# Kernel optimization log

Hardware: AMD Instinct MI355X
Metric: run time of the kernel (lower is better)

## Reference

```python
import jax, jax.numpy as jnp
import numpy as np
import math

EPS = 1e-15
R_CUT = 5.0
BERN_K = 16
FEAT = 128
N_ATOMS = 16384
N_EDGES = 100000
# log binomial(BERN_K-1, k) for the Bernstein radial basis
LOG_BINOM = np.array([math.lgamma(BERN_K) - math.lgamma(k + 1) - math.lgamma(BERN_K - k)
                      for k in range(BERN_K)], dtype=np.float32)


def swish(x, a, b):
    # learnable swish: a * x * sigmoid(b * x)
    return a * x * jax.nn.sigmoid(b * x)


def resmlp(x, W1, b1, W2, b2, Wout, aa, bb):
    # Residual( PreAct(lin1) -> PreAct(lin2) ) -> act -> Linear(no bias)
    h = swish(x, aa[0], bb[0]) @ W1.T + b1
    h = swish(h, aa[1], bb[1]) @ W2.T + b2
    y = x + h
    return swish(y, aa[2], bb[2]) @ Wout.T


def sph_harm(u, l):
    ux, uy, uz = u[:, 0], u[:, 1], u[:, 2]
    if l == 0:
        return jnp.ones((u.shape[0], 1), u.dtype)
    if l == 1:
        return jnp.stack([uy, uz, ux], axis=-1)
    s3 = 3.0 ** 0.5
    return jnp.stack([s3 * ux * uy, s3 * uy * uz, 0.5 * (3.0 * uz ** 2 - 1.0),
                      s3 * ux * uz, 0.5 * s3 * (ux ** 2 - uy ** 2)], axis=-1)


def bernstein_rho(r, gamma):
    # rho_k(r) = C(K-1,k) x^k (1-x)^(K-1-k) * f_cut(r), x = exp(-gamma r)
    k = jnp.arange(BERN_K, dtype=r.dtype)
    x = jnp.exp(-gamma * r)[:, None]                      # (E,1)
    bern = jnp.exp(jnp.asarray(LOG_BINOM)) * x ** k * (1.0 - x) ** (BERN_K - 1 - k)
    inside = r < R_CUT
    denom = jnp.where(inside, R_CUT ** 2 - r ** 2, 1.0)
    fcut = jnp.where(inside, jnp.exp(-r ** 2 / denom), 0.0)
    return bern * fcut[:, None]                           # (E,K)


def setup_inputs() -> dict:
    key = jax.random.key(0)
    ks = jax.random.split(key, 16)
    D, K = FEAT, BERN_K
    sc = 1.0 / (D ** 0.5)
    inp = {
        'xyz': jax.random.normal(ks[0], (N_ATOMS, 3), jnp.float32),
        'x_tilde': jax.random.normal(ks[1], (N_ATOMS, D), jnp.float32),
        'nbrs': jax.random.randint(ks[2], (N_EDGES, 2), 0, N_ATOMS),
        # 5 ResidualMLPs stacked: order [c, s, p, d, l]
        'W1': jax.random.normal(ks[3], (5, D, D), jnp.float32) * sc,
        'b1': jnp.zeros((5, D), jnp.float32),
        'W2': jax.random.normal(ks[4], (5, D, D), jnp.float32) * sc,
        'b2': jnp.zeros((5, D), jnp.float32),
        'Wout': jax.random.normal(ks[5], (5, D, D), jnp.float32) * sc,
        'act_a': jnp.ones((5, 3), jnp.float32),
        'act_b': jnp.full((5, 3), 1.702, jnp.float32),
        'G_s': jax.random.normal(ks[6], (D, K), jnp.float32) * (1.0 / K ** 0.5),
        'G_p': jax.random.normal(ks[7], (D, K), jnp.float32) * (1.0 / K ** 0.5),
        'G_d': jax.random.normal(ks[8], (D, K), jnp.float32) * (1.0 / K ** 0.5),
        'P_1': jax.random.normal(ks[9], (D, D), jnp.float32) * sc,
        'P_2': jax.random.normal(ks[10], (D, D), jnp.float32) * sc,
        'D_1': jax.random.normal(ks[11], (D, D), jnp.float32) * sc,
        'D_2': jax.random.normal(ks[12], (D, D), jnp.float32) * sc,
        'gamma': jnp.asarray(0.5, jnp.float32),
    }
    return inp


def reference(xyz, x_tilde, nbrs, W1, b1, W2, b2, Wout, act_a, act_b,
              G_s, G_p, G_d, P_1, P_2, D_1, D_2, gamma):
    N = xyz.shape[0]
    src = nbrs[:, 0]
    dst = nbrs[:, 1]
    r_ij = xyz[dst] - xyz[src]                            # (E,3)
    r = jnp.sqrt((r_ij ** 2 + EPS).sum(-1))               # stable norm, (E,)
    u = r_ij / r[:, None]
    rho = bernstein_rho(r, gamma)                         # (E,K)
    x_j = x_tilde[dst]                                    # (E,D)

    def mlp(x, i):
        return resmlp(x, W1[i], b1[i], W2[i], b2[i], Wout[i], act_a[i], act_b[i])

    c_term = mlp(x_tilde, 0)                              # (N,D)

    quants = []
    for i, (l, G) in enumerate([(0, G_s), (1, G_p), (2, G_d)]):
        y = sph_harm(u, l)                                # (E,M)
        # fused g_matmul: G @ (rho (x) y) -> (E,D,M), avoids (E,K,M) temp
        gm = jnp.einsum('dk,ek,em->edm', G, rho, y)
        feat = mlp(x_j, i + 1)                            # (E,D)
        per_nbr = feat[:, :, None] * gm                   # (E,D,M)
        quants.append(jax.ops.segment_sum(per_nbr, src, num_segments=N))

    def take_inner(q, M1, M2):
        t1 = jnp.einsum('ij,njm->nim', M1, q)
        t2 = jnp.einsum('ij,njm->nim', M2, q)
        return (t1 * t2).sum(-1)                          # (N,D)

    inp = c_term + quants[0][:, :, 0] \
        + take_inner(quants[1], P_1, P_2) + take_inner(quants[2], D_1, D_2)
    return mlp(inp, 4)
```

## Files before the change

kernel.cpp:

```cpp
#include <hip/hip_runtime.h>
#include <math.h>

#define D 128

typedef __attribute__((ext_vector_type(8))) short short8v;
typedef __attribute__((ext_vector_type(4))) float f32x4;
typedef __attribute__((ext_vector_type(4))) unsigned int uint4v;

__device__ __forceinline__ float fast_swish(float v, float a, float b) {
  float e = __builtin_amdgcn_exp2f(-1.4426950408889634f * (b * v));
  return a * v * __builtin_amdgcn_rcpf(1.0f + e);
}

__device__ __forceinline__ void bf16split_rne(float v, unsigned short& h, unsigned short& l) {
  unsigned int u = __float_as_uint(v);
  unsigned int rh = (u + 0x7FFFu + ((u >> 16) & 1u)) & 0xFFFF0000u;
  h = (unsigned short)(rh >> 16);
  float lf = v - __uint_as_float(rh);
  unsigned int u2 = __float_as_uint(lf);
  unsigned int rl = u2 + 0x7FFFu + ((u2 >> 16) & 1u);
  l = (unsigned short)(rl >> 16);
}

__device__ __forceinline__ void bf16split_fast(float v, unsigned short& h, unsigned short& l) {
  unsigned int u = __float_as_uint(v);
  h = (unsigned short)(u >> 16);
  float lf = v - __uint_as_float(u & 0xFFFF0000u);
  unsigned int u2 = __float_as_uint(lf);
  l = (unsigned short)((u2 + 0x7FFFu + ((u2 >> 16) & 1u)) >> 16);
}

__device__ __forceinline__ f32x4 mfma3(short8v ah, short8v al, short8v bh, short8v bl, f32x4 acc) {
  acc = __builtin_amdgcn_mfma_f32_16x16x32_bf16(al, bh, acc, 0, 0, 0);
  acc = __builtin_amdgcn_mfma_f32_16x16x32_bf16(ah, bl, acc, 0, 0, 0);
  acc = __builtin_amdgcn_mfma_f32_16x16x32_bf16(ah, bh, acc, 0, 0, 0);
  return acc;
}

template <bool SW>
__device__ __forceinline__ void stage16(const float* __restrict__ src, int lane,
                                        unsigned short* shHi, unsigned short* shLo,
                                        float a, float b) {
#pragma unroll
  for (int i = 0; i < 4; ++i) {
    int t = lane + 64 * i;
    int r = t >> 4, c = t & 15;
    const float4 v0 = *(const float4*)(src + r * D + c * 8);
    const float4 v1 = *(const float4*)(src + r * D + c * 8 + 4);
    float vv[8] = {v0.x, v0.y, v0.z, v0.w, v1.x, v1.y, v1.z, v1.w};
    unsigned int hw[4], lw[4];
#pragma unroll
    for (int jj = 0; jj < 4; ++jj) {
      float x0 = SW ? fast_swish(vv[2 * jj], a, b) : vv[2 * jj];
      float x1 = SW ? fast_swish(vv[2 * jj + 1], a, b) : vv[2 * jj + 1];
      unsigned short h0, l0, h1, l1;
      bf16split_fast(x0, h0, l0);
      bf16split_fast(x1, h1, l1);
      hw[jj] = (unsigned int)h0 | ((unsigned int)h1 << 16);
      lw[jj] = (unsigned int)l0 | ((unsigned int)l1 << 16);
    }
    int off = (c * 16) ^ ((r & 7) << 4);
    uint4v hv = {hw[0], hw[1], hw[2], hw[3]};
    uint4v lv = {lw[0], lw[1], lw[2], lw[3]};
    *(uint4v*)((char*)(shHi + r * D) + off) = hv;
    *(uint4v*)((char*)(shLo + r * D) + off) = lv;
  }
}

__global__ void prep_weights_kernel(const float* __restrict__ W1, const float* __restrict__ W2,
                                    const float* __restrict__ Wo, const float* __restrict__ P1,
                                    const float* __restrict__ P2, const float* __restrict__ D1,
                                    const float* __restrict__ D2, unsigned short* __restrict__ prep) {
  int t = blockIdx.x * 256 + threadIdx.x;
  if (t >= 19 * 2048) return;
  int m = t >> 11;
  int rem = t & 2047;
  int nt = rem >> 8;
  int kc = (rem >> 6) & 3;
  int lane = rem & 63;
  const float* src;
  if (m < 5) src = W1 + (size_t)m * 16384;
  else if (m < 10) src = W2 + (size_t)(m - 5) * 16384;
  else if (m < 15) src = Wo + (size_t)(m - 10) * 16384;
  else if (m == 15) src = P1;
  else if (m == 16) src = P2;
  else if (m == 17) src = D1;
  else src = D2;
  int row = nt * 16 + (lane & 15);
  int k0 = kc * 32 + (lane >> 4) * 8;
  unsigned int hw[4], lw[4];
#pragma unroll
  for (int jj = 0; jj < 4; ++jj) {
    unsigned short h0, l0, h1, l1;
    bf16split_rne(src[row * D + k0 + 2 * jj], h0, l0);
    bf16split_rne(src[row * D + k0 + 2 * jj + 1], h1, l1);
    hw[jj] = (unsigned int)h0 | ((unsigned int)h1 << 16);
    lw[jj] = (unsigned int)l0 | ((unsigned int)l1 << 16);
  }
  size_t chunk = (size_t)((nt * 4 + kc) * 64 + lane);
  uint4v hv = {hw[0], hw[1], hw[2], hw[3]};
  uint4v lv = {lw[0], lw[1], lw[2], lw[3]};
  *(uint4v*)(prep + (size_t)(2 * m) * 16384 + chunk * 8) = hv;
  *(uint4v*)(prep + (size_t)(2 * m + 1) * 16384 + chunk * 8) = lv;
}

__global__ __launch_bounds__(256) void resmlp_mfma(
    const float* __restrict__ xin, const unsigned short* __restrict__ prep,
    const float* __restrict__ b1b, const float* __restrict__ b2b,
    const float* __restrict__ act_a, const float* __restrict__ act_b,
    float* __restrict__ outbase, int branch_off, int n_atoms)
{
  __shared__ __align__(16) unsigned short shHi[64 * D];
  __shared__ __align__(16) unsigned short shLo[64 * D];
  const int lane = threadIdx.x & 63;
  const int wid = threadIdx.x >> 6;
  const int atom0 = blockIdx.x * 64;
  const int br = blockIdx.y + branch_off;
  const float* b1 = b1b + br * D;
  const float* b2 = b2b + br * D;
  const float a0 = act_a[br * 3 + 0], g0 = act_b[br * 3 + 0];
  const float a1 = act_a[br * 3 + 1], g1 = act_b[br * 3 + 1];
  const float a2 = act_a[br * 3 + 2], g2 = act_b[br * 3 + 2];
  float* out = outbase + (size_t)blockIdx.y * n_atoms * D;
  const float* x0 = xin + (size_t)atom0 * D;

  stage16<true>(x0 + wid * 16 * D, lane, shHi + wid * 16 * D, shLo + wid * 16 * D, a0, g0);
  __syncthreads();

  const int rl = lane & 15;
  const int q = lane >> 4;
  const int rowq = q * 4;
  const int nt0 = wid * 2;

  f32x4 acc[4][2];

#define GEMM_LAYER(mat)                                                        \
  do {                                                                         \
    const unsigned short* ph = prep + (size_t)(2 * (mat)) * 16384;             \
    const unsigned short* pl = prep + (size_t)(2 * (mat) + 1) * 16384;         \
    _Pragma("unroll") for (int mt = 0; mt < 4; ++mt)                           \
        _Pragma("unroll") for (int j = 0; j < 2; ++j)                          \
            acc[mt][j] = f32x4{0.f, 0.f, 0.f, 0.f};                            \
    _Pragma("unroll") for (int kc = 0; kc < 4; ++kc) {                         \
      int ci0 = (nt0 * 4 + kc) * 64 + lane;                                    \
      int ci1 = ((nt0 + 1) * 4 + kc) * 64 + lane;                              \
      short8v bh0 = *(const short8v*)(ph + (size_t)ci0 * 8);                   \
      short8v bl0 = *(const short8v*)(pl + (size_t)ci0 * 8);                   \
      short8v bh1 = *(const short8v*)(ph + (size_t)ci1 * 8);                   \
      short8v bl1 = *(const short8v*)(pl + (size_t)ci1 * 8);                   \
      int aoff = (kc * 64 + q * 16) ^ ((rl & 7) << 4);                         \
      _Pragma("unroll") for (int mt = 0; mt < 4; ++mt) {                       \
        short8v ah = *(const short8v*)((const char*)(shHi + (mt * 16 + rl) * D) + aoff); \
        short8v al = *(const short8v*)((const char*)(shLo + (mt * 16 + rl) * D) + aoff); \
        acc[mt][0] = mfma3(ah, al, bh0, bl0, acc[mt][0]);                      \
        acc[mt][1] = mfma3(ah, al, bh1, bl1, acc[mt][1]);                      \
      }                                                                        \
    }                                                                          \
  } while (0)

  GEMM_LAYER(br);
  __syncthreads();
#pragma unroll
  for (int j = 0; j < 2; ++j) {
    int col = (nt0 + j) * 16 + rl;
    float bv = b1[col];
#pragma unroll
    for (int mt = 0; mt < 4; ++mt)
#pragma unroll
      for (int r = 0; r < 4; ++r) {
        int row = mt * 16 + rowq + r;
        float s = fast_swish(acc[mt][j][r] + bv, a1, g1);
        unsigned short h, l;
        bf16split_fast(s, h, l);
        int off = (col * 2) ^ ((row & 7) << 4);
        *(unsigned short*)((char*)(shHi + row * D) + off) = h;
        *(unsigned short*)((char*)(shLo + row * D) + off) = l;
      }
  }
  __syncthreads();

  GEMM_LAYER(5 + br);
  __syncthreads();
#pragma unroll
  for (int j = 0; j < 2; ++j) {
    int col = (nt0 + j) * 16 + rl;
    float bv = b2[col];
#pragma unroll
    for (int mt = 0; mt < 4; ++mt)
#pragma unroll
      for (int r = 0; r < 4; ++r) {
        int row = mt * 16 + rowq + r;
        float y = x0[row * D + col] + acc[mt][j][r] + bv;
        float s = fast_swish(y, a2, g2);
        unsigned short h, l;
        bf16split_fast(s, h, l);
        int off = (col * 2) ^ ((row & 7) << 4);
        *(unsigned short*)((char*)(shHi + row * D) + off) = h;
        *(unsigned short*)((char*)(shLo + row * D) + off) = l;
      }
  }
  __syncthreads();

  GEMM_LAYER(10 + br);
#pragma unroll
  for (int j = 0; j < 2; ++j)
#pragma unroll
    for (int mt = 0; mt < 4; ++mt)
#pragma unroll
      for (int r = 0; r < 4; ++r)
        out[(size_t)(atom0 + mt * 16 + rowq + r) * D + (nt0 + j) * 16 + rl] = acc[mt][j][r];
#undef GEMM_LAYER
}

__global__ __launch_bounds__(256) void inner_mfma(
    const float* __restrict__ q1, const float* __restrict__ q2,
    const unsigned short* __restrict__ prep,
    float* __restrict__ pA, float* __restrict__ pB, int n_atoms)
{
  __shared__ __align__(16) unsigned short shHi[64 * D];
  __shared__ __align__(16) unsigned short shLo[64 * D];
  const int lane = threadIdx.x & 63;
  const int wid = threadIdx.x >> 6;
  const int atom0 = blockIdx.x * 64;
  const int g = blockIdx.y;
  const size_t nd = (size_t)n_atoms * D;
  const int rl = lane & 15;
  const int q = lane >> 4;
  const int rowq = q * 4;
  const int nt0 = wid * 2;

  f32x4 eacc[4][2];
#pragma unroll
  for (int mt = 0; mt < 4; ++mt)
#pragma unroll
    for (int j = 0; j < 2; ++j) eacc[mt][j] = f32x4{0.f, 0.f, 0.f, 0.f};

  for (int pp = 0; pp < 2; ++pp) {
    const int part = g * 2 + pp;
    const float* qp = (part < 3) ? q1 + (size_t)part * nd : q2 + (size_t)(part - 3) * nd;
    const int m1 = (part < 3) ? 15 : 17;
    if (pp) __syncthreads();
    stage16<false>(qp + (size_t)atom0 * D + wid * 16 * D, lane,
                   shHi + wid * 16 * D, shLo + wid * 16 * D, 0.f, 0.f);
    __syncthreads();
    const unsigned short* p1h = prep + (size_t)(2 * m1) * 16384;
    const unsigned short* p1l = prep + (size_t)(2 * m1 + 1) * 16384;
    const unsigned short* p2h = prep + (size_t)(2 * m1 + 2) * 16384;
    const unsigned short* p2l = prep + (size_t)(2 * m1 + 3) * 16384;
#pragma unroll
    for (int j = 0; j < 2; ++j) {
      f32x4 t1[4], t2[4];
#pragma unroll
      for (int mt = 0; mt < 4; ++mt) {
        t1[mt] = f32x4{0.f, 0.f, 0.f, 0.f};
        t2[mt] = f32x4{0.f, 0.f, 0.f, 0.f};
      }
#pragma unroll
      for (int kc = 0; kc < 4; ++kc) {
        int ci = ((nt0 + j) * 4 + kc) * 64 + lane;
        short8v b1h = *(const short8v*)(p1h + (size_t)ci * 8);
        short8v b1l = *(const short8v*)(p1l + (size_t)ci * 8);
        short8v b2h = *(const short8v*)(p2h + (size_t)ci * 8);
        short8v b2l = *(const short8v*)(p2l + (size_t)ci * 8);
        int aoff = (kc * 64 + q * 16) ^ ((rl & 7) << 4);
#pragma unroll
        for (int mt = 0; mt < 4; ++mt) {
          short8v ah = *(const short8v*)((const char*)(shHi + (mt * 16 + rl) * D) + aoff);
          short8v al = *(const short8v*)((const char*)(shLo + (mt * 16 + rl) * D) + aoff);
          t1[mt] = mfma3(ah, al, b1h, b1l, t1[mt]);
          t2[mt] = mfma3(ah, al, b2h, b2l, t2[mt]);
        }
      }
#pragma unroll
      for (int mt = 0; mt < 4; ++mt) eacc[mt][j] += t1[mt] * t2[mt];
    }
  }

  float* outp = (g < 3) ? (pA + (size_t)g * nd) : pB;
#pragma unroll
  for (int j = 0; j < 2; ++j)
#pragma unroll
    for (int mt = 0; mt < 4; ++mt)
#pragma unroll
      for (int r = 0; r < 4; ++r)
        outp[(size_t)(atom0 + mt * 16 + rowq + r) * D + (nt0 + j) * 16 + rl] = eacc[mt][j][r];
}

__global__ void edge_geom_kernel(const float* __restrict__ xyz,
                                 const int* __restrict__ nbrs,
                                 const float* __restrict__ gamma_p,
                                 float* __restrict__ rho_ws,
                                 float* __restrict__ y_ws, int n_edges)
{
  int e = blockIdx.x * 256 + threadIdx.x;
  if (e >= n_edges) return;
  int s = nbrs[2 * e], dd = nbrs[2 * e + 1];
  float rx = xyz[3 * dd + 0] - xyz[3 * s + 0];
  float ry = xyz[3 * dd + 1] - xyz[3 * s + 1];
  float rz = xyz[3 * dd + 2] - xyz[3 * s + 2];
  float r2 = rx * rx + ry * ry + rz * rz + 3e-15f;
  float r = sqrtf(r2);
  float inv = 1.0f / r;
  float ux = rx * inv, uy = ry * inv, uz = rz * inv;
  float gamma = gamma_p[0];
  float xv = __expf(-gamma * r);
  float omx = 1.0f - xv;
  float fcut = 0.0f;
  if (r < 5.0f) fcut = __expf(-r2 / (25.0f - r2));
  float xp[16], op[16];
  xp[0] = 1.f; op[0] = 1.f;
#pragma unroll
  for (int k = 1; k < 16; ++k) { xp[k] = xp[k - 1] * xv; op[k] = op[k - 1] * omx; }
  const float C[16] = {1.f, 15.f, 105.f, 455.f, 1365.f, 3003.f, 5005.f, 6435.f,
                       6435.f, 5005.f, 3003.f, 1365.f, 455.f, 105.f, 15.f, 1.f};
  float* rp = rho_ws + (size_t)e * 16;
#pragma unroll
  for (int k = 0; k < 16; ++k) rp[k] = C[k] * xp[k] * op[15 - k] * fcut;
  const float s3 = 1.7320508075688772f;
  float* yp = y_ws + (size_t)e * 8;
  yp[0] = uy; yp[1] = uz; yp[2] = ux;
  yp[3] = s3 * ux * uy; yp[4] = s3 * uy * uz; yp[5] = 0.5f * (3.f * uz * uz - 1.f);
  yp[6] = s3 * ux * uz; yp[7] = 0.5f * s3 * (ux * ux - uy * uy);
}

__global__ void hist_kernel(const int* __restrict__ nbrs, int* __restrict__ counts, int n_edges) {
  int e = blockIdx.x * 256 + threadIdx.x;
  if (e < n_edges) atomicAdd(&counts[nbrs[2 * e]], 1);
}

__global__ __launch_bounds__(1024) void scan_kernel(const int* __restrict__ counts,
                                                    int* __restrict__ offsets, int n) {
  __shared__ int part[1024];
  int tid = threadIdx.x;
  int base = tid * 16;
  int loc[16]; int s = 0;
#pragma unroll
  for (int i = 0; i < 16; ++i) {
    int c = (base + i < n) ? counts[base + i] : 0;
    loc[i] = c; s += c;
  }
  part[tid] = s;
  __syncthreads();
  for (int off = 1; off < 1024; off <<= 1) {
    int v = (tid >= off) ? part[tid - off] : 0;
    __syncthreads();
    part[tid] += v;
    __syncthreads();
  }
  int run = (tid == 0) ? 0 : part[tid - 1];
#pragma unroll
  for (int i = 0; i < 16; ++i) {
    if (base + i < n) offsets[base + i] = run;
    run += loc[i];
  }
}

__global__ void scatter_kernel(const int* __restrict__ nbrs, const int* __restrict__ offsets,
                               int* __restrict__ cursor, int* __restrict__ sorted, int n_edges) {
  int e = blockIdx.x * 256 + threadIdx.x;
  if (e < n_edges) {
    int s = nbrs[2 * e];
    int pos = offsets[s] + atomicAdd(&cursor[s], 1);
    sorted[pos] = e;
  }
}

__global__ __launch_bounds__(128) void aggregate_kernel(
    const float* __restrict__ rho_ws, const float* __restrict__ y_ws,
    const int* __restrict__ nbrs, const int* __restrict__ offsets,
    const int* __restrict__ counts, const int* __restrict__ sorted,
    const float* __restrict__ feat1, const float* __restrict__ feat2,
    const float* __restrict__ feat3,
    const float* __restrict__ Gs, const float* __restrict__ Gp,
    const float* __restrict__ Gd,
    float* __restrict__ q0, float* __restrict__ q1, float* __restrict__ q2,
    int n_atoms)
{
  int n = blockIdx.x;
  int d = threadIdx.x;
  float gs[16], gp[16], gd[16];
#pragma unroll
  for (int c = 0; c < 4; ++c) {
    float4 v = *(const float4*)&Gs[d * 16 + 4 * c];
    gs[4 * c] = v.x; gs[4 * c + 1] = v.y; gs[4 * c + 2] = v.z; gs[4 * c + 3] = v.w;
    v = *(const float4*)&Gp[d * 16 + 4 * c];
    gp[4 * c] = v.x; gp[4 * c + 1] = v.y; gp[4 * c + 2] = v.z; gp[4 * c + 3] = v.w;
    v = *(const float4*)&Gd[d * 16 + 4 * c];
    gd[4 * c] = v.x; gd[4 * c + 1] = v.y; gd[4 * c + 2] = v.z; gd[4 * c + 3] = v.w;
  }
  float a0 = 0.f, a1[3] = {0.f, 0.f, 0.f}, a2[5] = {0.f, 0.f, 0.f, 0.f, 0.f};
  int off = offsets[n], cnt = counts[n];
  for (int i = 0; i < cnt; ++i) {
    int e = sorted[off + i];
    int dst = nbrs[2 * e + 1];
    const float4* rp = (const float4*)(rho_ws + (size_t)e * 16);
    float4 r0v = rp[0], r1v = rp[1], r2v = rp[2], r3v = rp[3];
    float rho[16] = {r0v.x, r0v.y, r0v.z, r0v.w, r1v.x, r1v.y, r1v.z, r1v.w,
                     r2v.x, r2v.y, r2v.z, r2v.w, r3v.x, r3v.y, r3v.z, r3v.w};
    const float4* ypv = (const float4*)(y_ws + (size_t)e * 8);
    float4 y0v = ypv[0], y1v = ypv[1];
    float g_s = 0.f, g_p = 0.f, g_d = 0.f;
#pragma unroll
    for (int k = 0; k < 16; ++k) {
      g_s += gs[k] * rho[k];
      g_p += gp[k] * rho[k];
      g_d += gd[k] * rho[k];
    }
    float f1 = feat1[(size_t)dst * D + d];
    float f2 = feat2[(size_t)dst * D + d];
    float f3 = feat3[(size_t)dst * D + d];
    a0 += f1 * g_s;
    float ap = f2 * g_p;
    a1[0] += ap * y0v.x; a1[1] += ap * y0v.y; a1[2] += ap * y0v.z;
    float ad = f3 * g_d;
    a2[0] += ad * y0v.w; a2[1] += ad * y1v.x; a2[2] += ad * y1v.y;
    a2[3] += ad * y1v.z; a2[4] += ad * y1v.w;
  }
  q0[(size_t)n * D + d] = a0;
#pragma unroll
  for (int m = 0; m < 3; ++m) q1[((size_t)m * n_atoms + n) * D + d] = a1[m];
#pragma unroll
  for (int m = 0; m < 5; ++m) q2[((size_t)m * n_atoms + n) * D + d] = a2[m];
}

__global__ void assemble_kernel(const float* __restrict__ cterm,
                                const float* __restrict__ q0,
                                const float* __restrict__ pA,
                                const float* __restrict__ pB,
                                float* __restrict__ inp, int nd4)
{
  int i = blockIdx.x * 256 + threadIdx.x;
  if (i >= nd4) return;
  const float4* c = (const float4*)cterm;
  const float4* z = (const float4*)q0;
  const float4* a = (const float4*)pA;
  const float4* b = (const float4*)pB;
  float4 v = c[i], zz = z[i];
  float4 a0 = a[i], a1 = a[i + (size_t)nd4], a2 = a[i + 2 * (size_t)nd4], bb = b[i];
  float4 r;
  r.x = v.x + zz.x + a0.x + a1.x + a2.x + bb.x;
  r.y = v.y + zz.y + a0.y + a1.y + a2.y + bb.y;
  r.z = v.z + zz.z + a0.z + a1.z + a2.z + bb.z;
  r.w = v.w + zz.w + a0.w + a1.w + a2.w + bb.w;
  ((float4*)inp)[i] = r;
}

extern "C" void kernel_launch(void* const* d_in, const int* in_sizes, int n_in,
                              void* d_out, int out_size, void* d_ws, size_t ws_size,
                              hipStream_t stream)
{
  const float* xyz     = (const float*)d_in[0];
  const float* x_tilde = (const float*)d_in[1];
  const int*   nbrs    = (const int*)d_in[2];
  const float* W1      = (const float*)d_in[3];
  const float* b1      = (const float*)d_in[4];
  const float* W2      = (const float*)d_in[5];
  const float* b2      = (const float*)d_in[6];
  const float* Wout    = (const float*)d_in[7];
  const float* act_a   = (const float*)d_in[8];
  const float* act_b   = (const float*)d_in[9];
  const float* Gs      = (const float*)d_in[10];
  const float* Gp      = (const float*)d_in[11];
  const float* Gd      = (const float*)d_in[12];
  const float* P1      = (const float*)d_in[13];
  const float* P2      = (const float*)d_in[14];
  const float* D1m     = (const float*)d_in[15];
  const float* D2m     = (const float*)d_in[16];
  const float* gamma   = (const float*)d_in[17];
  float* out = (float*)d_out;

  const int n_atoms = in_sizes[0] / 3;
  const int n_edges = in_sizes[2] / 2;

  float* ws = (float*)d_ws;
  size_t nd = (size_t)n_atoms * D;
  float* feats  = ws;
  float* q0     = feats + 4 * nd;
  float* q1     = q0 + nd;
  float* q2     = q1 + 3 * nd;
  float* rho_ws = q2 + 5 * nd;
  float* y_ws   = rho_ws + (size_t)n_edges * 16;
  float* inp    = y_ws + (size_t)n_edges * 8;
  int* counts  = (int*)(inp + nd);
  int* offsets = counts + n_atoms;
  int* cursor  = offsets + n_atoms;
  int* sorted  = cursor + n_atoms;
  unsigned short* prep =
      (unsigned short*)(((uintptr_t)(sorted + n_edges) + 15) & ~(uintptr_t)15);

  float* pA = feats + nd;
  float* pB = rho_ws;

  hipMemsetAsync(counts, 0, (size_t)n_atoms * sizeof(int), stream);
  hipMemsetAsync(cursor, 0, (size_t)n_atoms * sizeof(int), stream);

  dim3 blk(256);
  int eb = (n_edges + 255) / 256;

  prep_weights_kernel<<<(19 * 2048 + 255) / 256, blk, 0, stream>>>(
      W1, W2, Wout, P1, P2, D1m, D2m, prep);

  resmlp_mfma<<<dim3(n_atoms / 64, 4), dim3(256), 0, stream>>>(
      x_tilde, prep, b1, b2, act_a, act_b, feats, 0, n_atoms);

  edge_geom_kernel<<<eb, blk, 0, stream>>>(xyz, nbrs, gamma, rho_ws, y_ws, n_edges);
  hist_kernel<<<eb, blk, 0, stream>>>(nbrs, counts, n_edges);
  scan_kernel<<<1, 1024, 0, stream>>>(counts, offsets, n_atoms);
  scatter_kernel<<<eb, blk, 0, stream>>>(nbrs, offsets, cursor, sorted, n_edges);

  aggregate_kernel<<<n_atoms, 128, 0, stream>>>(
      rho_ws, y_ws, nbrs, offsets, counts, sorted,
      feats + nd, feats + 2 * nd, feats + 3 * nd, Gs, Gp, Gd,
      q0, q1, q2, n_atoms);

  inner_mfma<<<dim3(n_atoms / 64, 4), dim3(256), 0, stream>>>(
      q1, q2, prep, pA, pB, n_atoms);

  assemble_kernel<<<(int)((nd / 4 + 255) / 256), blk, 0, stream>>>(
      feats, q0, pA, pB, inp, (int)(nd / 4));

  resmlp_mfma<<<dim3(n_atoms / 64, 1), dim3(256), 0, stream>>>(
      inp, prep, b1, b2, act_a, act_b, out, 4, n_atoms);
}
```

Measured before the change: 274.6 us.

## Fuse edge geometry into sorted scatter, interleave branch features, drop assemble kernel

Edge geometry (rho, spherical harmonics, destination index) is now computed inside the scatter kernel and written directly in source-sorted order, so aggregation streams records contiguously without the indirect sorted/nbrs lookups. The three edge-branch MLP outputs are interleaved per atom (384 floats) so one gather reads all three features. The separate assemble kernel is removed: the c-term is written to inp, aggregation adds q0 into it, and inner_mfma atomically adds its four partial inner products into inp. This removes a kernel launch and several full N×D intermediate round trips, at the cost of float atomics that make summation order nondeterministic and add contention across the 4 grid-y blocks.

```diff
diff --git a/kernel.cpp b/kernel.cpp
--- a/kernel.cpp
+++ b/kernel.cpp
@@ -108,20 +108,21 @@
     const float* __restrict__ xin, const unsigned short* __restrict__ prep,
     const float* __restrict__ b1b, const float* __restrict__ b2b,
     const float* __restrict__ act_a, const float* __restrict__ act_b,
-    float* __restrict__ outbase, int branch_off, int n_atoms)
+    float* __restrict__ outA, float* __restrict__ outB,
+    int branch_off, int n_atoms)
 {
   __shared__ __align__(16) unsigned short shHi[64 * D];
   __shared__ __align__(16) unsigned short shLo[64 * D];
   const int lane = threadIdx.x & 63;
   const int wid = threadIdx.x >> 6;
   const int atom0 = blockIdx.x * 64;
-  const int br = blockIdx.y + branch_off;
+  const int y = blockIdx.y;
+  const int br = y + branch_off;
   const float* b1 = b1b + br * D;
   const float* b2 = b2b + br * D;
   const float a0 = act_a[br * 3 + 0], g0 = act_b[br * 3 + 0];
   const float a1 = act_a[br * 3 + 1], g1 = act_b[br * 3 + 1];
   const float a2 = act_a[br * 3 + 2], g2 = act_b[br * 3 + 2];
-  float* out = outbase + (size_t)blockIdx.y * n_atoms * D;
   const float* x0 = xin + (size_t)atom0 * D;
 
   stage16<true>(x0 + wid * 16 * D, lane, shHi + wid * 16 * D, shLo + wid * 16 * D, a0, g0);
@@ -190,8 +191,8 @@
 #pragma unroll
       for (int r = 0; r < 4; ++r) {
         int row = mt * 16 + rowq + r;
-        float y = x0[row * D + col] + acc[mt][j][r] + bv;
-        float s = fast_swish(y, a2, g2);
+        float yv = x0[row * D + col] + acc[mt][j][r] + bv;
+        float s = fast_swish(yv, a2, g2);
         unsigned short h, l;
         bf16split_fast(s, h, l);
         int off = (col * 2) ^ ((row & 7) << 4);
@@ -203,19 +204,23 @@
 
   GEMM_LAYER(10 + br);
 #pragma unroll
-  for (int j = 0; j < 2; ++j)
-#pragma unroll
-    for (int mt = 0; mt < 4; ++mt)
-#pragma unroll
-      for (int r = 0; r < 4; ++r)
-        out[(size_t)(atom0 + mt * 16 + rowq + r) * D + (nt0 + j) * 16 + rl] = acc[mt][j][r];
+  for (int mt = 0; mt < 4; ++mt)
+#pragma unroll
+    for (int r = 0; r < 4; ++r) {
+      int row = atom0 + mt * 16 + rowq + r;
+      float* op = (y == 0) ? (outA + (size_t)row * D)
+                           : (outB + ((size_t)row * 3 + (y - 1)) * D);
+#pragma unroll
+      for (int j = 0; j < 2; ++j)
+        op[(nt0 + j) * 16 + rl] = acc[mt][j][r];
+    }
 #undef GEMM_LAYER
 }
 
 __global__ __launch_bounds__(256) void inner_mfma(
     const float* __restrict__ q1, const float* __restrict__ q2,
     const unsigned short* __restrict__ prep,
-    float* __restrict__ pA, float* __restrict__ pB, int n_atoms)
+    float* __restrict__ inp, int n_atoms)
 {
   __shared__ __align__(16) unsigned short shHi[64 * D];
   __shared__ __align__(16) unsigned short shLo[64 * D];
@@ -276,25 +281,60 @@
     }
   }
 
-  float* outp = (g < 3) ? (pA + (size_t)g * nd) : pB;
 #pragma unroll
   for (int j = 0; j < 2; ++j)
 #pragma unroll
     for (int mt = 0; mt < 4; ++mt)
 #pragma unroll
       for (int r = 0; r < 4; ++r)
-        outp[(size_t)(atom0 + mt * 16 + rowq + r) * D + (nt0 + j) * 16 + rl] = eacc[mt][j][r];
-}
-
-__global__ void edge_geom_kernel(const float* __restrict__ xyz,
-                                 const int* __restrict__ nbrs,
-                                 const float* __restrict__ gamma_p,
-                                 float* __restrict__ rho_ws,
-                                 float* __restrict__ y_ws, int n_edges)
+        atomicAdd(&inp[(size_t)(atom0 + mt * 16 + rowq + r) * D + (nt0 + j) * 16 + rl],
+                  eacc[mt][j][r]);
+}
+
+__global__ void hist_kernel(const int* __restrict__ nbrs, int* __restrict__ counts, int n_edges) {
+  int e = blockIdx.x * 256 + threadIdx.x;
+  if (e < n_edges) atomicAdd(&counts[nbrs[2 * e]], 1);
+}
+
+__global__ __launch_bounds__(1024) void scan_kernel(const int* __restrict__ counts,
+                                                    int* __restrict__ offsets, int n) {
+  __shared__ int part[1024];
+  int tid = threadIdx.x;
+  int base = tid * 16;
+  int loc[16]; int s = 0;
+#pragma unroll
+  for (int i = 0; i < 16; ++i) {
+    int c = (base + i < n) ? counts[base + i] : 0;
+    loc[i] = c; s += c;
+  }
+  part[tid] = s;
+  __syncthreads();
+  for (int off = 1; off < 1024; off <<= 1) {
+    int v = (tid >= off) ? part[tid - off] : 0;
+    __syncthreads();
+    part[tid] += v;
+    __syncthreads();
+  }
+  int run = (tid == 0) ? 0 : part[tid - 1];
+#pragma unroll
+  for (int i = 0; i < 16; ++i) {
+    if (base + i < n) offsets[base + i] = run;
+    run += loc[i];
+  }
+}
+
+__global__ void scatter_geom_kernel(const float* __restrict__ xyz,
+                                    const int* __restrict__ nbrs,
+                                    const float* __restrict__ gamma_p,
+                                    const int* __restrict__ offsets,
+                                    int* __restrict__ cursor,
+                                    float* __restrict__ rho_s, float* __restrict__ y_s,
+                                    int* __restrict__ dst_s, int n_edges)
 {
   int e = blockIdx.x * 256 + threadIdx.x;
   if (e >= n_edges) return;
   int s = nbrs[2 * e], dd = nbrs[2 * e + 1];
+  int pos = offsets[s] + atomicAdd(&cursor[s], 1);
   float rx = xyz[3 * dd + 0] - xyz[3 * s + 0];
   float ry = xyz[3 * dd + 1] - xyz[3 * s + 1];
   float rz = xyz[3 * dd + 2] - xyz[3 * s + 2];
@@ -313,67 +353,31 @@
   for (int k = 1; k < 16; ++k) { xp[k] = xp[k - 1] * xv; op[k] = op[k - 1] * omx; }
   const float C[16] = {1.f, 15.f, 105.f, 455.f, 1365.f, 3003.f, 5005.f, 6435.f,
                        6435.f, 5005.f, 3003.f, 1365.f, 455.f, 105.f, 15.f, 1.f};
-  float* rp = rho_ws + (size_t)e * 16;
-#pragma unroll
-  for (int k = 0; k < 16; ++k) rp[k] = C[k] * xp[k] * op[15 - k] * fcut;
+  float* rp = rho_s + (size_t)pos * 16;
+#pragma unroll
+  for (int c4 = 0; c4 < 4; ++c4) {
+    float4 v = make_float4(C[4 * c4] * xp[4 * c4] * op[15 - 4 * c4] * fcut,
+                           C[4 * c4 + 1] * xp[4 * c4 + 1] * op[14 - 4 * c4] * fcut,
+                           C[4 * c4 + 2] * xp[4 * c4 + 2] * op[13 - 4 * c4] * fcut,
+                           C[4 * c4 + 3] * xp[4 * c4 + 3] * op[12 - 4 * c4] * fcut);
+    *(float4*)(rp + 4 * c4) = v;
+  }
   const float s3 = 1.7320508075688772f;
-  float* yp = y_ws + (size_t)e * 8;
-  yp[0] = uy; yp[1] = uz; yp[2] = ux;
-  yp[3] = s3 * ux * uy; yp[4] = s3 * uy * uz; yp[5] = 0.5f * (3.f * uz * uz - 1.f);
-  yp[6] = s3 * ux * uz; yp[7] = 0.5f * s3 * (ux * ux - uy * uy);
-}
-
-__global__ void hist_kernel(const int* __restrict__ nbrs, int* __restrict__ counts, int n_edges) {
-  int e = blockIdx.x * 256 + threadIdx.x;
-  if (e < n_edges) atomicAdd(&counts[nbrs[2 * e]], 1);
-}
-
-__global__ __launch_bounds__(1024) void scan_kernel(const int* __restrict__ counts,
-                                                    int* __restrict__ offsets, int n) {
-  __shared__ int part[1024];
-  int tid = threadIdx.x;
-  int base = tid * 16;
-  int loc[16]; int s = 0;
-#pragma unroll
-  for (int i = 0; i < 16; ++i) {
-    int c = (base + i < n) ? counts[base + i] : 0;
-    loc[i] = c; s += c;
-  }
-  part[tid] = s;
-  __syncthreads();
-  for (int off = 1; off < 1024; off <<= 1) {
-    int v = (tid >= off) ? part[tid - off] : 0;
-    __syncthreads();
-    part[tid] += v;
-    __syncthreads();
-  }
-  int run = (tid == 0) ? 0 : part[tid - 1];
-#pragma unroll
-  for (int i = 0; i < 16; ++i) {
-    if (base + i < n) offsets[base + i] = run;
-    run += loc[i];
-  }
-}
-
-__global__ void scatter_kernel(const int* __restrict__ nbrs, const int* __restrict__ offsets,
-                               int* __restrict__ cursor, int* __restrict__ sorted, int n_edges) {
-  int e = blockIdx.x * 256 + threadIdx.x;
-  if (e < n_edges) {
-    int s = nbrs[2 * e];
-    int pos = offsets[s] + atomicAdd(&cursor[s], 1);
-    sorted[pos] = e;
-  }
+  float* yp = y_s + (size_t)pos * 8;
+  *(float4*)yp = make_float4(uy, uz, ux, s3 * ux * uy);
+  *(float4*)(yp + 4) = make_float4(s3 * uy * uz, 0.5f * (3.f * uz * uz - 1.f),
+                                   s3 * ux * uz, 0.5f * s3 * (ux * ux - uy * uy));
+  dst_s[pos] = dd;
 }
 
 __global__ __launch_bounds__(128) void aggregate_kernel(
-    const float* __restrict__ rho_ws, const float* __restrict__ y_ws,
-    const int* __restrict__ nbrs, const int* __restrict__ offsets,
-    const int* __restrict__ counts, const int* __restrict__ sorted,
-    const float* __restrict__ feat1, const float* __restrict__ feat2,
-    const float* __restrict__ feat3,
+    const float* __restrict__ rho_s, const float* __restrict__ y_s,
+    const int* __restrict__ dst_s,
+    const int* __restrict__ offsets, const int* __restrict__ counts,
+    const float* __restrict__ featsI,
     const float* __restrict__ Gs, const float* __restrict__ Gp,
     const float* __restrict__ Gd,
-    float* __restrict__ q0, float* __restrict__ q1, float* __restrict__ q2,
+    float* __restrict__ inp, float* __restrict__ q1, float* __restrict__ q2,
     int n_atoms)
 {
   int n = blockIdx.x;
@@ -389,60 +393,48 @@
     gd[4 * c] = v.x; gd[4 * c + 1] = v.y; gd[4 * c + 2] = v.z; gd[4 * c + 3] = v.w;
   }
   float a0 = 0.f, a1[3] = {0.f, 0.f, 0.f}, a2[5] = {0.f, 0.f, 0.f, 0.f, 0.f};
-  int off = offsets[n], cnt = counts[n];
-  for (int i = 0; i < cnt; ++i) {
-    int e = sorted[off + i];
-    int dst = nbrs[2 * e + 1];
-    const float4* rp = (const float4*)(rho_ws + (size_t)e * 16);
-    float4 r0v = rp[0], r1v = rp[1], r2v = rp[2], r3v = rp[3];
-    float rho[16] = {r0v.x, r0v.y, r0v.z, r0v.w, r1v.x, r1v.y, r1v.z, r1v.w,
-                     r2v.x, r2v.y, r2v.z, r2v.w, r3v.x, r3v.y, r3v.z, r3v.w};
-    const float4* ypv = (const float4*)(y_ws + (size_t)e * 8);
-    float4 y0v = ypv[0], y1v = ypv[1];
-    float g_s = 0.f, g_p = 0.f, g_d = 0.f;
-#pragma unroll
-    for (int k = 0; k < 16; ++k) {
-      g_s += gs[k] * rho[k];
-      g_p += gp[k] * rho[k];
-      g_d += gd[k] * rho[k];
-    }
-    float f1 = feat1[(size_t)dst * D + d];
-    float f2 = feat2[(size_t)dst * D + d];
-    float f3 = feat3[(size_t)dst * D + d];
-    a0 += f1 * g_s;
-    float ap = f2 * g_p;
-    a1[0] += ap * y0v.x; a1[1] += ap * y0v.y; a1[2] += ap * y0v.z;
-    float ad = f3 * g_d;
-    a2[0] += ad * y0v.w; a2[1] += ad * y1v.x; a2[2] += ad * y1v.y;
-    a2[3] += ad * y1v.z; a2[4] += ad * y1v.w;
-  }
-  q0[(size_t)n * D + d] = a0;
+  const int off = offsets[n], cnt = counts[n];
+
+#define EDGE_BODY(REC)                                                         \
+  do {                                                                         \
+    const int rec = (REC);                                                     \
+    const int dst = dst_s[rec];                                                \
+    const float* fb = featsI + (size_t)dst * 384;                              \
+    float f1 = fb[d], f2 = fb[128 + d], f3 = fb[256 + d];                      \
+    const float4* rp = (const float4*)(rho_s + (size_t)rec * 16);              \
+    float4 r0v = rp[0], r1v = rp[1], r2v = rp[2], r3v = rp[3];                 \
+    float rho[16] = {r0v.x, r0v.y, r0v.z, r0v.w, r1v.x, r1v.y, r1v.z, r1v.w,   \
+                     r2v.x, r2v.y, r2v.z, r2v.w, r3v.x, r3v.y, r3v.z, r3v.w};  \
+    const float4* ypv = (const float4*)(y_s + (size_t)rec * 8);                \
+    float4 y0v = ypv[0], y1v = ypv[1];                                         \
+    float g_s = 0.f, g_p = 0.f, g_d = 0.f;                                     \
+    _Pragma("unroll") for (int k = 0; k < 16; ++k) {                           \
+      g_s += gs[k] * rho[k];                                                   \
+      g_p += gp[k] * rho[k];                                                   \
+      g_d += gd[k] * rho[k];                                                   \
+    }                                                                          \
+    a0 += f1 * g_s;                                                            \
+    float ap = f2 * g_p;                                                       \
+    a1[0] += ap * y0v.x; a1[1] += ap * y0v.y; a1[2] += ap * y0v.z;             \
+    float ad = f3 * g_d;                                                       \
+    a2[0] += ad * y0v.w; a2[1] += ad * y1v.x; a2[2] += ad * y1v.y;             \
+    a2[3] += ad * y1v.z; a2[4] += ad * y1v.w;                                  \
+  } while (0)
+
+  int i = 0;
+  for (; i + 2 <= cnt; i += 2) {
+    EDGE_BODY(off + i);
+    EDGE_BODY(off + i + 1);
+  }
+  if (i < cnt) EDGE_BODY(off + i);
+#undef EDGE_BODY
+
+  size_t idx = (size_t)n * D + d;
+  inp[idx] = inp[idx] + a0;
 #pragma unroll
   for (int m = 0; m < 3; ++m) q1[((size_t)m * n_atoms + n) * D + d] = a1[m];
 #pragma unroll
   for (int m = 0; m < 5; ++m) q2[((size_t)m * n_atoms + n) * D + d] = a2[m];
-}
-
-__global__ void assemble_kernel(const float* __restrict__ cterm,
-                                const float* __restrict__ q0,
-                                const float* __restrict__ pA,
-                                const float* __restrict__ pB,
-                                float* __restrict__ inp, int nd4)
-{
-  int i = blockIdx.x * 256 + threadIdx.x;
-  if (i >= nd4) return;
-  const float4* c = (const float4*)cterm;
-  const float4* z = (const float4*)q0;
-  const float4* a = (const float4*)pA;
-  const float4* b = (const float4*)pB;
-  float4 v = c[i], zz = z[i];
-  float4 a0 = a[i], a1 = a[i + (size_t)nd4], a2 = a[i + 2 * (size_t)nd4], bb = b[i];
-  float4 r;
-  r.x = v.x + zz.x + a0.x + a1.x + a2.x + bb.x;
-  r.y = v.y + zz.y + a0.y + a1.y + a2.y + bb.y;
-  r.z = v.z + zz.z + a0.z + a1.z + a2.z + bb.z;
-  r.w = v.w + zz.w + a0.w + a1.w + a2.w + bb.w;
-  ((float4*)inp)[i] = r;
 }
 
 extern "C" void kernel_launch(void* const* d_in, const int* in_sizes, int n_in,
@@ -474,25 +466,20 @@
 
   float* ws = (float*)d_ws;
   size_t nd = (size_t)n_atoms * D;
-  float* feats  = ws;
-  float* q0     = feats + 4 * nd;
-  float* q1     = q0 + nd;
+  float* featsI = ws;
+  float* q1     = featsI + 3 * nd;
   float* q2     = q1 + 3 * nd;
-  float* rho_ws = q2 + 5 * nd;
-  float* y_ws   = rho_ws + (size_t)n_edges * 16;
-  float* inp    = y_ws + (size_t)n_edges * 8;
-  int* counts  = (int*)(inp + nd);
+  float* inp    = q2 + 5 * nd;
+  float* rho_s  = inp + nd;
+  float* y_s    = rho_s + (size_t)n_edges * 16;
+  int* dst_s   = (int*)(y_s + (size_t)n_edges * 8);
+  int* counts  = dst_s + n_edges;
   int* offsets = counts + n_atoms;
   int* cursor  = offsets + n_atoms;
-  int* sorted  = cursor + n_atoms;
   unsigned short* prep =
-      (unsigned short*)(((uintptr_t)(sorted + n_edges) + 15) & ~(uintptr_t)15);
-
-  float* pA = feats + nd;
-  float* pB = rho_ws;
-
-  hipMemsetAsync(counts, 0, (size_t)n_atoms * sizeof(int), stream);
-  hipMemsetAsync(cursor, 0, (size_t)n_atoms * sizeof(int), stream);
+      (unsigned short*)(((uintptr_t)(cursor + n_atoms) + 15) & ~(uintptr_t)15);
+
+  hipMemsetAsync(counts, 0, (size_t)3 * n_atoms * sizeof(int), stream);
 
   dim3 blk(256);
   int eb = (n_edges + 255) / 256;
@@ -501,24 +488,20 @@
       W1, W2, Wout, P1, P2, D1m, D2m, prep);
 
   resmlp_mfma<<<dim3(n_atoms / 64, 4), dim3(256), 0, stream>>>(
-      x_tilde, prep, b1, b2, act_a, act_b, feats, 0, n_atoms);
-
-  edge_geom_kernel<<<eb, blk, 0, stream>>>(xyz, nbrs, gamma, rho_ws, y_ws, n_edges);
+      x_tilde, prep, b1, b2, act_a, act_b, inp, featsI, 0, n_atoms);
+
   hist_kernel<<<eb, blk, 0, stream>>>(nbrs, counts, n_edges);
   scan_kernel<<<1, 1024, 0, stream>>>(counts, offsets, n_atoms);
-  scatter_kernel<<<eb, blk, 0, stream>>>(nbrs, offsets, cursor, sorted, n_edges);
+  scatter_geom_kernel<<<eb, blk, 0, stream>>>(
+      xyz, nbrs, gamma, offsets, cursor, rho_s, y_s, dst_s, n_edges);
 
   aggregate_kernel<<<n_atoms, 128, 0, stream>>>(
-      rho_ws, y_ws, nbrs, offsets, counts, sorted,
-      feats + nd, feats + 2 * nd, feats + 3 * nd, Gs, Gp, Gd,
-      q0, q1, q2, n_atoms);
+      rho_s, y_s, dst_s, offsets, counts, featsI, Gs, Gp, Gd,
+      inp, q1, q2, n_atoms);
 
   inner_mfma<<<dim3(n_atoms / 64, 4), dim3(256), 0, stream>>>(
-      q1, q2, prep, pA, pB, n_atoms);
-
-  assemble_kernel<<<(int)((nd / 4 + 255) / 256), blk, 0, stream>>>(
-      feats, q0, pA, pB, inp, (int)(nd / 4));
+      q1, q2, prep, inp, n_atoms);
 
   resmlp_mfma<<<dim3(n_atoms / 64, 1), dim3(256), 0, stream>>>(
-      inp, prep, b1, b2, act_a, act_b, out, 4, n_atoms);
-}
+      inp, prep, b1, b2, act_a, act_b, out, nullptr, 4, n_atoms);
+}
```

Result: slower. 283.2 us (+3.1%).
